# Kernel tuning notes

Measured on AMD Instinct MI355X. Metric: run time of the kernel, lower is better.

## Reference

```python
import jax, jax.numpy as jnp
import numpy as np

B, C, F, K = 16, 1000, 256, 10
IPM_ITERS = 20   # fixed-iteration primal-dual interior point (qpth eps=0.01 analogue)
SIGMA = 0.1      # centering parameter
MARGIN = 0.05


def setup_inputs() -> dict:
    key = jax.random.key(0)
    ks = jax.random.split(key, 6)
    logits_pred = jax.random.normal(ks[0], (B, C), jnp.float32)
    feats_pred = jax.random.normal(ks[1], (B, F), jnp.float32)
    feats_pred_0 = jax.random.normal(ks[2], (B, F), jnp.float32)
    head_W = jax.random.normal(ks[3], (C, F), jnp.float32) * 0.05
    head_bias = jax.random.normal(ks[4], (C,), jnp.float32) * 0.05
    # K distinct attack-target classes per sample (order defines the desired ranking)
    perm = jax.vmap(lambda k: jax.random.permutation(k, C))(jax.random.split(ks[5], B))
    attack_targets = perm[:, :K].astype(jnp.int32)
    margin = jnp.full((1,), MARGIN, jnp.float32)
    return {"logits_pred": logits_pred, "feats_pred": feats_pred,
            "feats_pred_0": feats_pred_0, "attack_targets": attack_targets,
            "head_W": head_W, "head_bias": head_bias, "margin": margin}


def build_D(attack_targets):
    # replicates the torch scatter/index_put sequence, in the same overwrite order
    col = jnp.arange(C)
    t_last = attack_targets[:, -1]
    base = -jnp.eye(C, dtype=jnp.float32)[None]                       # (B,C,C) via broadcast
    D = jnp.where(col[None, None, :] == t_last[:, None, None], 1.0, base)
    row_mask = (jnp.arange(C)[None, :, None] == attack_targets[:, None, :]).any(-1)  # (B,C)
    D = jnp.where(row_mask[:, :, None], 0.0, D)
    bi = jnp.broadcast_to(jnp.arange(B)[:, None], (B, K - 1))
    t_pos = attack_targets[:, :-1]
    t_neg = attack_targets[:, 1:]
    D = D.at[bi, t_neg, t_neg].set(-1.0)
    D = D.at[bi, t_neg, t_pos].set(1.0)
    return D


def solve_qp_ipm(p, G, h):
    # min_z z'z + p'z  s.t. G z <= h   (Q = 2*I), infeasible-start primal-dual IPM
    Bn, m, n = G.shape
    z = -0.5 * p                       # unconstrained minimizer (anchor feats)
    s = jnp.ones((Bn, m), p.dtype)
    lam = jnp.ones((Bn, m), p.dtype)
    eye_n = jnp.eye(n, dtype=p.dtype)
    big = jnp.asarray(1e10, p.dtype)

    def step(carry, _):
        z, lam, s = carry
        mu = (lam * s).mean(-1, keepdims=True)
        rd = 2.0 * z + p + jnp.einsum('bm,bmn->bn', lam, G)
        rp = jnp.einsum('bmn,bn->bm', G, z) + s - h
        rc = lam * s - SIGMA * mu
        w = lam / s
        M = 2.0 * eye_n + jnp.einsum('bmi,bm,bmj->bij', G, w, G)   # (B,n,n) KKT Schur
        rhs = -(rd + jnp.einsum('bmi,bm->bi', G, (lam * rp - rc) / s))
        dz = jnp.linalg.solve(M, rhs[..., None])[..., 0]
        ds = -rp - jnp.einsum('bmn,bn->bm', G, dz)
        dlam = -(rc + lam * ds) / s
        a1 = jnp.where(ds < 0, -s / ds, big).min(-1)
        a2 = jnp.where(dlam < 0, -lam / dlam, big).min(-1)
        alpha = jnp.minimum(1.0, 0.99 * jnp.minimum(a1, a2))[:, None]
        return (z + alpha * dz, lam + alpha * dlam, s + alpha * ds), None

    (z, lam, s), _ = jax.lax.scan(step, (z, lam, s), None, length=IPM_ITERS)
    return z


def reference(logits_pred, feats_pred, feats_pred_0, attack_targets, head_W, head_bias, margin):
    D = build_D(attack_targets)                                   # (B,C,C)
    G = -jnp.einsum('bck,kf->bcf', D, head_W)                     # (B,C,F)
    Hc = jnp.einsum('bck,k->bc', D, head_bias) - margin[0]        # = -(margin - D@b)
    Hc = Hc.at[jnp.arange(B), attack_targets[:, 0]].set(0.0)
    P = -2.0 * feats_pred
    z_sol = solve_qp_ipm(P, G, Hc)
    loss = ((feats_pred - z_sol) ** 2).sum(-1)                    # (B,)
    return loss
```

## Files before the change

### kernel.cpp

```cpp
#include <hip/hip_runtime.h>


#define B_N 16
#define C_N 1000
#define F_N 256
#define ITERS_N 20
#define SIGMA_C 0.1f
#define BIGV 1e10f

static const size_t OFF_WT  = 0;
static const size_t OFF_X   = 256000;
static const size_t OFF_M64 = 4352000;
static const size_t OFF_H   = 6449152;
static const size_t OFF_LAM = OFF_H   + 16000;
static const size_t OFF_S   = OFF_LAM + 16000;
static const size_t OFF_RP  = OFF_S   + 16000;
static const size_t OFF_RC  = OFF_RP  + 16000;
static const size_t OFF_WV  = OFF_RC  + 16000;
static const size_t OFF_Z   = OFF_WV  + 16000;
static const size_t OFF_DZ  = OFF_Z   + 4096;
static const size_t OFF_RHS = OFF_DZ  + 4096;
static const size_t OFF_AI  = OFF_RHS + 4096;
static const size_t OFF_BI  = OFF_AI  + 16000;

__device__ __forceinline__ float bsum256(float v, float* red) {
#pragma unroll
  for (int o = 32; o > 0; o >>= 1) v += __shfl_down(v, o);
  __syncthreads();
  if ((threadIdx.x & 63) == 0) red[threadIdx.x >> 6] = v;
  __syncthreads();
  return red[0] + red[1] + red[2] + red[3];
}
__device__ __forceinline__ float bmin256(float v, float* red) {
#pragma unroll
  for (int o = 32; o > 0; o >>= 1) v = fminf(v, __shfl_down(v, o));
  __syncthreads();
  if ((threadIdx.x & 63) == 0) red[threadIdx.x >> 6] = v;
  __syncthreads();
  return fminf(fminf(red[0], red[1]), fminf(red[2], red[3]));
}

__global__ __launch_bounds__(256) void k_transpose(const float* __restrict__ W,
                                                   float* __restrict__ WT) {
  __shared__ float tile[64][65];
  int tc = blockIdx.x & 15, tk = blockIdx.x >> 4;
  int c0 = tc * 64, k0 = tk * 64;
  int t = threadIdx.x;
  int jj = t & 63, r4 = t >> 6;
#pragma unroll
  for (int i = 0; i < 16; ++i) {
    int r = r4 + i * 4;
    int c = c0 + r;
    tile[r][jj] = (c < C_N) ? W[c * F_N + k0 + jj] : 0.f;
  }
  __syncthreads();
#pragma unroll
  for (int i = 0; i < 16; ++i) {
    int kr = r4 + i * 4;
    int cc = c0 + jj;
    if (cc < C_N) WT[(k0 + kr) * C_N + cc] = tile[jj][kr];
  }
}

__global__ __launch_bounds__(256) void k_setup(const int* __restrict__ tg,
                                               const float* __restrict__ bias,
                                               const float* __restrict__ feats,
                                               const float* __restrict__ marg,
                                               float* wsf) {
  int b = blockIdx.x, t = threadIdx.x;
  __shared__ int tsh[10];
  if (t < 10) tsh[t] = tg[b * 10 + t];
  __syncthreads();
  float m = marg[0];
  int t9 = tsh[9];
  float bias_t9 = bias[t9];
  int*   ai  = (int*)(wsf + OFF_AI) + b * C_N;
  int*   bi  = (int*)(wsf + OFF_BI) + b * C_N;
  float* h   = wsf + OFF_H   + b * C_N;
  float* lam = wsf + OFF_LAM + b * C_N;
  float* s   = wsf + OFF_S   + b * C_N;
#pragma unroll
  for (int r = 0; r < 4; ++r) {
    int c = t + 256 * r;
    if (c < C_N) {
      int rk = -1;
#pragma unroll
      for (int i = 0; i < 10; ++i) if (c == tsh[i]) rk = i;
      int av, bv; float hv;
      if (rk < 0)       { av = c;        bv = t9;         hv = bias_t9 - bias[c] - m; }
      else if (rk == 0) { av = 0;        bv = 0;          hv = 0.f; }
      else              { av = tsh[rk];  bv = tsh[rk-1];  hv = bias[tsh[rk-1]] - bias[tsh[rk]] - m; }
      ai[c] = av; bi[c] = bv; h[c] = hv; lam[c] = 1.f; s[c] = 1.f;
    }
  }
  (wsf + OFF_Z)[b * F_N + t] = feats[b * F_N + t];
}

__global__ __launch_bounds__(256) void k_buildX(const float* __restrict__ W,
                                                float* wsf) {
  int bb = blockIdx.x >> 3, part = blockIdx.x & 7;
  int t = threadIdx.x;
  __shared__ int aL[125], bL[125];
  int c0 = part * 125;
  const int* ai = (const int*)(wsf + OFF_AI) + bb * C_N;
  const int* bi = (const int*)(wsf + OFF_BI) + bb * C_N;
  if (t < 125) { aL[t] = ai[c0 + t]; bL[t] = bi[c0 + t]; }
  __syncthreads();
  float* X = wsf + OFF_X + (size_t)bb * 256000 + (size_t)c0 * F_N;
  for (int i = 0; i < 125; ++i) {
    float wa = W[aL[i] * F_N + t];
    float wb = W[bL[i] * F_N + t];
    X[i * F_N + t] = wa - wb;
  }
}

__global__ __launch_bounds__(256) void k_iter_pre(const float* __restrict__ W,
                                                  const float* __restrict__ feats,
                                                  const int* __restrict__ tg,
                                                  float* wsf, int do_update) {
  int b = blockIdx.x, t = threadIdx.x;
  __shared__ float zs[256], dzs[256];
  __shared__ __align__(16) float ys[1000];
  __shared__ float vs[1000];
  __shared__ float red[4];
  __shared__ int tsh[10];

  const float* WT = wsf + OFF_WT;
  const int* ai  = (const int*)(wsf + OFF_AI) + b * C_N;
  const int* bi  = (const int*)(wsf + OFF_BI) + b * C_N;
  float* h    = wsf + OFF_H   + b * C_N;
  float* lam  = wsf + OFF_LAM + b * C_N;
  float* s    = wsf + OFF_S   + b * C_N;
  float* rp   = wsf + OFF_RP  + b * C_N;
  float* rc   = wsf + OFF_RC  + b * C_N;
  float* wbuf = wsf + OFF_WV  + b * C_N;
  float* z    = wsf + OFF_Z   + b * F_N;
  float* dz   = wsf + OFF_DZ  + b * F_N;
  float* rhs  = wsf + OFF_RHS + b * F_N;

  if (t < 10) tsh[t] = tg[b * 10 + t];
  zs[t] = z[t];
  if (do_update) dzs[t] = dz[t];
  __syncthreads();

  float lamr[4], sr[4], rpr[4];
  if (do_update) {
    if (t < 250) {
      float4 acc = make_float4(0.f, 0.f, 0.f, 0.f);
      const float4* WT4 = (const float4*)WT;
#pragma unroll 4
      for (int k = 0; k < 256; ++k) {
        float zk = dzs[k];
        float4 w4 = WT4[k * 250 + t];
        acc.x += zk * w4.x; acc.y += zk * w4.y; acc.z += zk * w4.z; acc.w += zk * w4.w;
      }
      *(float4*)&ys[4 * t] = acc;
    }
    __syncthreads();
    float amin = BIGV;
    float dsr[4], dlr[4];
#pragma unroll
    for (int r = 0; r < 4; ++r) {
      int c = t + 256 * r;
      if (c < C_N) {
        float lv = lam[c], sv = s[c], rpv = rp[c], rcv = rc[c];
        float g = ys[ai[c]] - ys[bi[c]];
        float dsv = -rpv - g;
        float dlv = -(rcv + lv * dsv) / sv;
        if (dsv < 0.f) amin = fminf(amin, -sv / dsv);
        if (dlv < 0.f) amin = fminf(amin, -lv / dlv);
        lamr[r] = lv; sr[r] = sv; dsr[r] = dsv; dlr[r] = dlv;
      }
    }
    float am = bmin256(amin, red);
    float alpha = fminf(1.f, 0.99f * am);
#pragma unroll
    for (int r = 0; r < 4; ++r) {
      int c = t + 256 * r;
      if (c < C_N) {
        lamr[r] += alpha * dlr[r];
        sr[r]   += alpha * dsr[r];
        lam[c] = lamr[r]; s[c] = sr[r];
      }
    }
    zs[t] += alpha * dzs[t];
    z[t] = zs[t];
    __syncthreads();
  } else {
#pragma unroll
    for (int r = 0; r < 4; ++r) {
      int c = t + 256 * r;
      if (c < C_N) { lamr[r] = lam[c]; sr[r] = s[c]; }
    }
  }

  if (t < 250) {
    float4 acc = make_float4(0.f, 0.f, 0.f, 0.f);
    const float4* WT4 = (const float4*)WT;
#pragma unroll 4
    for (int k = 0; k < 256; ++k) {
      float zk = zs[k];
      float4 w4 = WT4[k * 250 + t];
      acc.x += zk * w4.x; acc.y += zk * w4.y; acc.z += zk * w4.z; acc.w += zk * w4.w;
    }
    *(float4*)&ys[4 * t] = acc;
  }
  __syncthreads();

  float musum = 0.f;
#pragma unroll
  for (int r = 0; r < 4; ++r) {
    int c = t + 256 * r;
    if (c < C_N) {
      float g = ys[ai[c]] - ys[bi[c]];
      rpr[r] = g + sr[r] - h[c];
      musum += lamr[r] * sr[r];
    }
  }
  float mu = bsum256(musum, red) * (1.f / 1000.f);

  float vsum = 0.f;
#pragma unroll
  for (int r = 0; r < 4; ++r) {
    int c = t + 256 * r;
    if (c < C_N) {
      float prod = lamr[r] * sr[r];
      float rcv = prod - SIGMA_C * mu;
      rc[c] = rcv; rp[c] = rpr[r];
      wbuf[c] = lamr[r] / sr[r];
      float vv = lamr[r] + (lamr[r] * rpr[r] - rcv) / sr[r];
      vs[c] = vv; vsum += vv;
    }
  }
  float S_all = bsum256(vsum, red);

  float vt[10];
#pragma unroll
  for (int i = 0; i < 10; ++i) vt[i] = vs[tsh[i]];
  float S_tgt = 0.f;
#pragma unroll
  for (int i = 0; i < 10; ++i) S_tgt += vt[i];
  float S_gen = S_all - S_tgt;
  __syncthreads();

#pragma unroll
  for (int r = 0; r < 4; ++r) {
    int c = t + 256 * r;
    if (c < C_N) {
      int rk = -1;
#pragma unroll
      for (int i = 0; i < 10; ++i) if (c == tsh[i]) rk = i;
      float vc = vs[c];
      float u;
      if (rk < 0)        u = vc;
      else if (rk == 0)  u = -vt[1];
      else if (rk < 9)   u = vc - vt[rk + 1];
      else               u = vc - S_gen;
      vs[c] = u;
    }
  }
  __syncthreads();

  {
    float acc = 0.f;
#pragma unroll 4
    for (int c = 0; c < C_N; ++c) acc += vs[c] * W[c * F_N + t];
    rhs[t] = -(2.f * zs[t] - 2.f * feats[b * F_N + t] + acc);
  }
}

__global__ __launch_bounds__(256) void k_syrk(float* wsf) {
  int blk = blockIdx.x;
  int b = blk / 10, tile = blk % 10;
  const int TI[10] = {0,1,1,2,2,2,3,3,3,3};
  const int TJ[10] = {0,0,1,0,1,2,0,1,2,3};
  int ti = TI[tile], tj = TJ[tile];
  int t = threadIdx.x;
  int tx = t & 15, ty = t >> 4;
  __shared__ __align__(16) float As[64][64];
  __shared__ __align__(16) float Bs[64][64];
  const float* X  = wsf + OFF_X  + (size_t)b * 256000;
  const float* wv = wsf + OFF_WV + b * C_N;
  float acc[4][4] = {{0.f}};
  int f4 = t & 15, jr0 = t >> 4;
  for (int cc = 0; cc < C_N; cc += 64) {
    __syncthreads();
#pragma unroll
    for (int rep = 0; rep < 4; ++rep) {
      int j = jr0 + rep * 16;
      int c = cc + j;
      float wj = (c < C_N) ? wv[c] : 0.f;
      float4 v = (c < C_N) ? *(const float4*)&X[(size_t)c * F_N + ti * 64 + f4 * 4]
                           : make_float4(0.f, 0.f, 0.f, 0.f);
      float4 u;
      if (tj == ti) u = v;
      else u = (c < C_N) ? *(const float4*)&X[(size_t)c * F_N + tj * 64 + f4 * 4]
                         : make_float4(0.f, 0.f, 0.f, 0.f);
      float4 vw = make_float4(wj * v.x, wj * v.y, wj * v.z, wj * v.w);
      *(float4*)&As[j][f4 * 4] = vw;
      *(float4*)&Bs[j][f4 * 4] = u;
    }
    __syncthreads();
#pragma unroll 4
    for (int j = 0; j < 64; ++j) {
      float4 a4 = *(const float4*)&As[j][tx * 4];
      float4 b4 = *(const float4*)&Bs[j][ty * 4];
      acc[0][0] += a4.x * b4.x; acc[0][1] += a4.x * b4.y; acc[0][2] += a4.x * b4.z; acc[0][3] += a4.x * b4.w;
      acc[1][0] += a4.y * b4.x; acc[1][1] += a4.y * b4.y; acc[1][2] += a4.y * b4.z; acc[1][3] += a4.y * b4.w;
      acc[2][0] += a4.z * b4.x; acc[2][1] += a4.z * b4.y; acc[2][2] += a4.z * b4.z; acc[2][3] += a4.z * b4.w;
      acc[3][0] += a4.w * b4.x; acc[3][1] += a4.w * b4.y; acc[3][2] += a4.w * b4.z; acc[3][3] += a4.w * b4.w;
    }
  }
  double* M64 = (double*)(wsf + OFF_M64) + (size_t)b * 65536;
#pragma unroll
  for (int e = 0; e < 4; ++e) {
    int i = ti * 64 + tx * 4 + e;
    int k0 = tj * 64 + ty * 4;
#pragma unroll
    for (int q = 0; q < 4; ++q) {
      float v = acc[e][q] + ((i == k0 + q) ? 2.f : 0.f);
      M64[(size_t)i * F_N + k0 + q] = (double)v;
    }
  }
}

__global__ __launch_bounds__(1024, 4) void k_chol(float* wsf) {
  int b = blockIdx.x, t = threadIdx.x;
  double* M = (double*)(wsf + OFF_M64) + (size_t)b * 65536;
  __shared__ double Sm[8464];
  double* Db   = Sm;
  double* invd = Sm + 272;
  double* Pb   = Sm + 304;
  double* Pu   = Sm + 4384;
  __shared__ double yv[256];
  __shared__ double red2[16 * 65];

  for (int p = 0; p < 16; ++p) {
    int p0 = p * 16, p1 = p0 + 16, nb = 256 - p1;

    if (t < 16) {
      int l = t;
      double a[16];
#pragma unroll
      for (int q = 0; q < 16; ++q) a[q] = M[(size_t)(p0 + l) * F_N + p0 + q];
#pragma unroll
      for (int j = 0; j < 16; ++j) {
        double d = __shfl(a[j], j);
        double dc = (fabs(d) < 1e-30) ? (d < 0.0 ? -1e-30 : 1e-30) : d;
        double inv = 1.0 / dc;
        if (l == j) a[j] = dc;
        else if (l > j) a[j] *= inv;
#pragma unroll
        for (int k = j + 1; k < 16; ++k) {
          double lkj = __shfl(a[j], k);
          if (l >= k) a[k] -= a[j] * (lkj * dc);
        }
      }
#pragma unroll
      for (int q = 0; q < 16; ++q) {
        M[(size_t)(p0 + l) * F_N + p0 + q] = a[q];
        Db[l * 17 + q] = a[q];
      }
      invd[l] = 1.0 / a[l];
    }
    __syncthreads();

    if (t < nb) {
      int r = p1 + t;
      double x[16];
#pragma unroll
      for (int q = 0; q < 16; ++q) x[q] = M[(size_t)r * F_N + p0 + q];
#pragma unroll
      for (int k = 0; k < 16; ++k) {
        double uk = x[k];
#pragma unroll
        for (int j = k + 1; j < 16; ++j) x[j] -= uk * Db[j * 17 + k];
        x[k] = uk * invd[k];
        Pu[t * 17 + k] = uk;
        Pb[t * 17 + k] = x[k];
      }
#pragma unroll
      for (int q = 0; q < 16; ++q) M[(size_t)r * F_N + p0 + q] = x[q];
    }
    __syncthreads();

    int nt4 = nb >> 2;
    int Ntile = nt4 * (nt4 + 1) / 2;
    for (int tt = t; tt < Ntile; tt += 1024) {
      float fsq = sqrtf((float)(8 * tt + 1));
      int ti = (int)((fsq - 1.f) * 0.5f);
      while ((ti + 1) * (ti + 2) / 2 <= tt) ++ti;
      while (ti * (ti + 1) / 2 > tt) --ti;
      int tk = tt - ti * (ti + 1) / 2;
      int ib = ti * 4, kb = tk * 4;
      double* m0 = M + (size_t)(p1 + ib) * F_N + p1 + kb;
      double a00 = m0[0],   a01 = m0[1],   a02 = m0[2],   a03 = m0[3];
      double a10 = m0[256], a11 = m0[257], a12 = m0[258], a13 = m0[259];
      double a20 = m0[512], a21 = m0[513], a22 = m0[514], a23 = m0[515];
      double a30 = m0[768], a31 = m0[769], a32 = m0[770], a33 = m0[771];
#pragma unroll
      for (int j = 0; j < 16; ++j) {
        double A0 = Pb[(ib + 0) * 17 + j], A1 = Pb[(ib + 1) * 17 + j];
        double A2 = Pb[(ib + 2) * 17 + j], A3 = Pb[(ib + 3) * 17 + j];
        double B0 = Pu[(kb + 0) * 17 + j], B1 = Pu[(kb + 1) * 17 + j];
        double B2 = Pu[(kb + 2) * 17 + j], B3 = Pu[(kb + 3) * 17 + j];
        a00 -= A0 * B0; a01 -= A0 * B1; a02 -= A0 * B2; a03 -= A0 * B3;
        a10 -= A1 * B0; a11 -= A1 * B1; a12 -= A1 * B2; a13 -= A1 * B3;
        a20 -= A2 * B0; a21 -= A2 * B1; a22 -= A2 * B2; a23 -= A2 * B3;
        a30 -= A3 * B0; a31 -= A3 * B1; a32 -= A3 * B2; a33 -= A3 * B3;
      }
      m0[0]   = a00; m0[1]   = a01; m0[2]   = a02; m0[3]   = a03;
      m0[256] = a10; m0[257] = a11; m0[258] = a12; m0[259] = a13;
      m0[512] = a20; m0[513] = a21; m0[514] = a22; m0[515] = a23;
      m0[768] = a30; m0[769] = a31; m0[770] = a32; m0[771] = a33;
    }
    __syncthreads();
  }

  {
    const float* rhs = wsf + OFF_RHS + (size_t)b * F_N;
    if (t < 256) yv[t] = (double)rhs[t];
  }
  __syncthreads();
  double* Ls = Sm;

  for (int blk = 0; blk < 4; ++blk) {
    int r0 = blk * 64;
    {
      int row = t >> 4, c4 = (t & 15) * 4;
#pragma unroll
      for (int q = 0; q < 4; ++q)
        Ls[row * 66 + c4 + q] = M[(size_t)(r0 + row) * F_N + r0 + c4 + q];
    }
    __syncthreads();
    if (t < 64) {
      int l = t;
      double acc = yv[r0 + l];
#pragma unroll
      for (int j = 0; j < 64; ++j) {
        double xj = __shfl(acc, j);
        if (l > j) acc -= Ls[l * 66 + j] * xj;
      }
      yv[r0 + l] = acc;
    }
    __syncthreads();
    int nrem = 192 - blk * 64;
    if (t < nrem) {
      int r = r0 + 64 + t;
      double a2 = 0.0;
#pragma unroll 4
      for (int j = 0; j < 64; ++j) a2 += M[(size_t)r * F_N + r0 + j] * yv[r0 + j];
      yv[r] -= a2;
    }
    __syncthreads();
  }

  if (t < 256) yv[t] = yv[t] / M[(size_t)t * F_N + t];
  __syncthreads();

  for (int blk = 3; blk >= 0; --blk) {
    int r0 = blk * 64, r1 = r0 + 64;
    if (blk < 3) {
      int i = r0 + (t & 63), g = t >> 6;
      double part = 0.0;
      for (int j = r1 + g; j < 256; j += 16) part += M[(size_t)j * F_N + i] * yv[j];
      red2[g * 65 + (t & 63)] = part;
      __syncthreads();
      if (t < 64) {
        double tot = 0.0;
#pragma unroll
        for (int g2 = 0; g2 < 16; ++g2) tot += red2[g2 * 65 + t];
        yv[r0 + t] -= tot;
      }
      __syncthreads();
    }
    {
      int row = t >> 4, c4 = (t & 15) * 4;
#pragma unroll
      for (int q = 0; q < 4; ++q)
        Ls[row * 66 + c4 + q] = M[(size_t)(r0 + row) * F_N + r0 + c4 + q];
    }
    __syncthreads();
    if (t < 64) {
      int l = t;
      double acc = yv[r0 + l];
#pragma unroll
      for (int j = 63; j >= 0; --j) {
        double xj = __shfl(acc, j);
        if (l < j) acc -= Ls[j * 66 + l] * xj;
      }
      yv[r0 + l] = acc;
    }
    __syncthreads();
  }

  if (t < 256) (wsf + OFF_DZ)[(size_t)b * F_N + t] = (float)yv[t];
}

__global__ __launch_bounds__(256) void k_final(const float* __restrict__ feats,
                                               float* wsf, float* __restrict__ out) {
  int b = blockIdx.x, t = threadIdx.x;
  __shared__ float zs[256], dzs[256];
  __shared__ __align__(16) float ys[1000];
  __shared__ float red[4];
  const float* WT = wsf + OFF_WT;
  const int* ai  = (const int*)(wsf + OFF_AI) + b * C_N;
  const int* bi  = (const int*)(wsf + OFF_BI) + b * C_N;
  const float* lam = wsf + OFF_LAM + b * C_N;
  const float* s   = wsf + OFF_S   + b * C_N;
  const float* rp  = wsf + OFF_RP  + b * C_N;
  const float* rc  = wsf + OFF_RC  + b * C_N;
  const float* z   = wsf + OFF_Z   + b * F_N;
  const float* dz  = wsf + OFF_DZ  + b * F_N;

  zs[t] = z[t];
  dzs[t] = dz[t];
  __syncthreads();
  if (t < 250) {
    float4 acc = make_float4(0.f, 0.f, 0.f, 0.f);
    const float4* WT4 = (const float4*)WT;
#pragma unroll 4
    for (int k = 0; k < 256; ++k) {
      float zk = dzs[k];
      float4 w4 = WT4[k * 250 + t];
      acc.x += zk * w4.x; acc.y += zk * w4.y; acc.z += zk * w4.z; acc.w += zk * w4.w;
    }
    *(float4*)&ys[4 * t] = acc;
  }
  __syncthreads();
  float amin = BIGV;
#pragma unroll
  for (int r = 0; r < 4; ++r) {
    int c = t + 256 * r;
    if (c < C_N) {
      float lv = lam[c], sv = s[c], rpv = rp[c], rcv = rc[c];
      float g = ys[ai[c]] - ys[bi[c]];
      float dsv = -rpv - g;
      float dlv = -(rcv + lv * dsv) / sv;
      if (dsv < 0.f) amin = fminf(amin, -sv / dsv);
      if (dlv < 0.f) amin = fminf(amin, -lv / dlv);
    }
  }
  float am = bmin256(amin, red);
  float alpha = fminf(1.f, 0.99f * am);
  float zf = zs[t] + alpha * dzs[t];
  float d = feats[b * F_N + t] - zf;
  float loss = bsum256(d * d, red);
  if (t == 0) out[b] = loss;
}

extern "C" void kernel_launch(void* const* d_in, const int* in_sizes, int n_in,
                              void* d_out, int out_size, void* d_ws, size_t ws_size,
                              hipStream_t stream) {
  (void)in_sizes; (void)n_in; (void)out_size; (void)ws_size;
  const float* feats = (const float*)d_in[1];
  const int*   tg    = (const int*)d_in[3];
  const float* W     = (const float*)d_in[4];
  const float* bias  = (const float*)d_in[5];
  const float* marg  = (const float*)d_in[6];
  float* wsf = (float*)d_ws;
  float* out = (float*)d_out;

  k_transpose<<<64, 256, 0, stream>>>(W, wsf + OFF_WT);
  k_setup<<<B_N, 256, 0, stream>>>(tg, bias, feats, marg, wsf);
  k_buildX<<<B_N * 8, 256, 0, stream>>>(W, wsf);
  for (int it = 0; it < ITERS_N; ++it) {
    k_iter_pre<<<B_N, 256, 0, stream>>>(W, feats, tg, wsf, it > 0 ? 1 : 0);
    k_syrk<<<B_N * 10, 256, 0, stream>>>(wsf);
    k_chol<<<B_N, 1024, 0, stream>>>(wsf);
  }
  k_final<<<B_N, 256, 0, stream>>>(feats, wsf, out);
}
```

Baseline: 8.466 ms.

## Overlap Cholesky panel factorization with trailing update via lookahead and double-buffered panels

Restructures the blocked LDL/Cholesky in k_chol to use lookahead. The next panel's column blocks are updated first, then the diagonal factorization and the triangular solve run on a few threads while the remaining threads update the rest of the trailing matrix. Panel buffers and inverse diagonals are double-buffered. Only the unscaled panel is stored, with the D^-1 scaling applied on the fly and an XOR swizzle on shared-memory rows to reduce bank conflicts. The aim is to cut the serial latency of the small diag/trsm phases, at the cost of more complex work partitioning and some extra multiplies in the update.

```diff
diff --git a/kernel.cpp b/kernel.cpp
--- a/kernel.cpp
+++ b/kernel.cpp
@@ -324,95 +324,142 @@
   }
 }
 
+#define PUROW(P, r, j) (P)[(r) * 17 + ((j) ^ ((r) & 7))]
+
+__device__ __forceinline__ void diag16(double* M, int P0d, double* Db,
+                                       double* invd) {
+  int l = threadIdx.x;
+  double a[16];
+#pragma unroll
+  for (int q = 0; q < 16; ++q) a[q] = M[(size_t)(P0d + l) * F_N + P0d + q];
+#pragma unroll
+  for (int j = 0; j < 16; ++j) {
+    double d = __shfl(a[j], j);
+    double dc = (fabs(d) < 1e-30) ? (d < 0.0 ? -1e-30 : 1e-30) : d;
+    double inv = 1.0 / dc;
+    if (l == j) a[j] = dc;
+    else if (l > j) a[j] *= inv;
+#pragma unroll
+    for (int k = j + 1; k < 16; ++k) {
+      double lkj = __shfl(a[j], k);
+      if (l >= k) a[k] -= a[j] * (lkj * dc);
+    }
+  }
+#pragma unroll
+  for (int q = 0; q < 16; ++q) {
+    M[(size_t)(P0d + l) * F_N + P0d + q] = a[q];
+    Db[l * 17 + q] = a[q];
+  }
+  invd[l] = 1.0 / a[l];
+}
+
+__device__ __forceinline__ void trsm16(double* M, int P0d, int tr,
+                                       const double* Db, const double* invd,
+                                       double* PuB) {
+  int r = P0d + 16 + tr;
+  double x[16];
+#pragma unroll
+  for (int q = 0; q < 16; ++q) x[q] = M[(size_t)r * F_N + P0d + q];
+#pragma unroll
+  for (int k = 0; k < 16; ++k) {
+    double uk = x[k];
+#pragma unroll
+    for (int j = k + 1; j < 16; ++j) x[j] -= uk * Db[j * 17 + k];
+    x[k] = uk * invd[k];
+    PUROW(PuB, tr, k) = uk;
+  }
+#pragma unroll
+  for (int q = 0; q < 16; ++q) M[(size_t)r * F_N + P0d + q] = x[q];
+}
+
+__device__ __forceinline__ void ldl_tile(double* M, const double* Pc,
+                                         const double* ic, int P1,
+                                         int ti, int tk) {
+  int ib = ti * 4, kb = tk * 4;
+  double* m0 = M + (size_t)(P1 + ib) * F_N + P1 + kb;
+  double a00 = m0[0],   a01 = m0[1],   a02 = m0[2],   a03 = m0[3];
+  double a10 = m0[256], a11 = m0[257], a12 = m0[258], a13 = m0[259];
+  double a20 = m0[512], a21 = m0[513], a22 = m0[514], a23 = m0[515];
+  double a30 = m0[768], a31 = m0[769], a32 = m0[770], a33 = m0[771];
+#pragma unroll
+  for (int j = 0; j < 16; ++j) {
+    double dj = ic[j];
+    double A0 = PUROW(Pc, ib + 0, j) * dj;
+    double A1 = PUROW(Pc, ib + 1, j) * dj;
+    double A2 = PUROW(Pc, ib + 2, j) * dj;
+    double A3 = PUROW(Pc, ib + 3, j) * dj;
+    double B0 = PUROW(Pc, kb + 0, j);
+    double B1 = PUROW(Pc, kb + 1, j);
+    double B2 = PUROW(Pc, kb + 2, j);
+    double B3 = PUROW(Pc, kb + 3, j);
+    a00 -= A0 * B0; a01 -= A0 * B1; a02 -= A0 * B2; a03 -= A0 * B3;
+    a10 -= A1 * B0; a11 -= A1 * B1; a12 -= A1 * B2; a13 -= A1 * B3;
+    a20 -= A2 * B0; a21 -= A2 * B1; a22 -= A2 * B2; a23 -= A2 * B3;
+    a30 -= A3 * B0; a31 -= A3 * B1; a32 -= A3 * B2; a33 -= A3 * B3;
+  }
+  m0[0]   = a00; m0[1]   = a01; m0[2]   = a02; m0[3]   = a03;
+  m0[256] = a10; m0[257] = a11; m0[258] = a12; m0[259] = a13;
+  m0[512] = a20; m0[513] = a21; m0[514] = a22; m0[515] = a23;
+  m0[768] = a30; m0[769] = a31; m0[770] = a32; m0[771] = a33;
+}
+
+__device__ __forceinline__ int2 trimap(int q) {
+  float fsq = sqrtf((float)(8 * q + 1));
+  int ti = (int)((fsq - 1.f) * 0.5f);
+  while ((ti + 1) * (ti + 2) / 2 <= q) ++ti;
+  while (ti * (ti + 1) / 2 > q) --ti;
+  return make_int2(ti, q - ti * (ti + 1) / 2);
+}
+
 __global__ __launch_bounds__(1024, 4) void k_chol(float* wsf) {
   int b = blockIdx.x, t = threadIdx.x;
   double* M = (double*)(wsf + OFF_M64) + (size_t)b * 65536;
   __shared__ double Sm[8464];
-  double* Db   = Sm;
-  double* invd = Sm + 272;
-  double* Pb   = Sm + 304;
-  double* Pu   = Sm + 4384;
   __shared__ double yv[256];
   __shared__ double red2[16 * 65];
-
-  for (int p = 0; p < 16; ++p) {
-    int p0 = p * 16, p1 = p0 + 16, nb = 256 - p1;
+  double* Db    = Sm;
+  double* invd2 = Sm + 272;
+  double* Pu    = Sm + 304;
+
+  if (t < 16) diag16(M, 0, Db, invd2);
+  __syncthreads();
+  if (t < 240) trsm16(M, 0, t, Db, invd2, Pu);
+  __syncthreads();
+
+  for (int p = 0; p < 15; ++p) {
+    int P1 = 16 * (p + 1);
+    int nt4 = (256 - P1) >> 2;
+    int m = nt4 - 4;
+    int N2 = m * (m + 1) / 2;
+    int Q = N2 > 768 ? N2 - 768 : 0;
+    int cur = p & 1, nxt = (p + 1) & 1;
+    const double* Pc = Pu + cur * 4080;
+    const double* ic = invd2 + cur * 16;
+
+    for (int q = t; q < 4 * nt4; q += 1024) {
+      int ti = q >> 2, tk = q & 3;
+      if (tk <= ti) ldl_tile(M, Pc, ic, P1, ti, tk);
+    }
+    __syncthreads();
 
     if (t < 16) {
-      int l = t;
-      double a[16];
-#pragma unroll
-      for (int q = 0; q < 16; ++q) a[q] = M[(size_t)(p0 + l) * F_N + p0 + q];
-#pragma unroll
-      for (int j = 0; j < 16; ++j) {
-        double d = __shfl(a[j], j);
-        double dc = (fabs(d) < 1e-30) ? (d < 0.0 ? -1e-30 : 1e-30) : d;
-        double inv = 1.0 / dc;
-        if (l == j) a[j] = dc;
-        else if (l > j) a[j] *= inv;
-#pragma unroll
-        for (int k = j + 1; k < 16; ++k) {
-          double lkj = __shfl(a[j], k);
-          if (l >= k) a[k] -= a[j] * (lkj * dc);
-        }
-      }
-#pragma unroll
-      for (int q = 0; q < 16; ++q) {
-        M[(size_t)(p0 + l) * F_N + p0 + q] = a[q];
-        Db[l * 17 + q] = a[q];
-      }
-      invd[l] = 1.0 / a[l];
-    }
-    __syncthreads();
-
-    if (t < nb) {
-      int r = p1 + t;
-      double x[16];
-#pragma unroll
-      for (int q = 0; q < 16; ++q) x[q] = M[(size_t)r * F_N + p0 + q];
-#pragma unroll
-      for (int k = 0; k < 16; ++k) {
-        double uk = x[k];
-#pragma unroll
-        for (int j = k + 1; j < 16; ++j) x[j] -= uk * Db[j * 17 + k];
-        x[k] = uk * invd[k];
-        Pu[t * 17 + k] = uk;
-        Pb[t * 17 + k] = x[k];
-      }
-#pragma unroll
-      for (int q = 0; q < 16; ++q) M[(size_t)r * F_N + p0 + q] = x[q];
-    }
-    __syncthreads();
-
-    int nt4 = nb >> 2;
-    int Ntile = nt4 * (nt4 + 1) / 2;
-    for (int tt = t; tt < Ntile; tt += 1024) {
-      float fsq = sqrtf((float)(8 * tt + 1));
-      int ti = (int)((fsq - 1.f) * 0.5f);
-      while ((ti + 1) * (ti + 2) / 2 <= tt) ++ti;
-      while (ti * (ti + 1) / 2 > tt) --ti;
-      int tk = tt - ti * (ti + 1) / 2;
-      int ib = ti * 4, kb = tk * 4;
-      double* m0 = M + (size_t)(p1 + ib) * F_N + p1 + kb;
-      double a00 = m0[0],   a01 = m0[1],   a02 = m0[2],   a03 = m0[3];
-      double a10 = m0[256], a11 = m0[257], a12 = m0[258], a13 = m0[259];
-      double a20 = m0[512], a21 = m0[513], a22 = m0[514], a23 = m0[515];
-      double a30 = m0[768], a31 = m0[769], a32 = m0[770], a33 = m0[771];
-#pragma unroll
-      for (int j = 0; j < 16; ++j) {
-        double A0 = Pb[(ib + 0) * 17 + j], A1 = Pb[(ib + 1) * 17 + j];
-        double A2 = Pb[(ib + 2) * 17 + j], A3 = Pb[(ib + 3) * 17 + j];
-        double B0 = Pu[(kb + 0) * 17 + j], B1 = Pu[(kb + 1) * 17 + j];
-        double B2 = Pu[(kb + 2) * 17 + j], B3 = Pu[(kb + 3) * 17 + j];
-        a00 -= A0 * B0; a01 -= A0 * B1; a02 -= A0 * B2; a03 -= A0 * B3;
-        a10 -= A1 * B0; a11 -= A1 * B1; a12 -= A1 * B2; a13 -= A1 * B3;
-        a20 -= A2 * B0; a21 -= A2 * B1; a22 -= A2 * B2; a23 -= A2 * B3;
-        a30 -= A3 * B0; a31 -= A3 * B1; a32 -= A3 * B2; a33 -= A3 * B3;
-      }
-      m0[0]   = a00; m0[1]   = a01; m0[2]   = a02; m0[3]   = a03;
-      m0[256] = a10; m0[257] = a11; m0[258] = a12; m0[259] = a13;
-      m0[512] = a20; m0[513] = a21; m0[514] = a22; m0[515] = a23;
-      m0[768] = a30; m0[769] = a31; m0[770] = a32; m0[771] = a33;
+      diag16(M, P1, Db, invd2 + nxt * 16);
+    } else if (t >= 64) {
+      for (int q = t - 64; q < Q; q += 960) {
+        int2 tt = trimap(q);
+        ldl_tile(M, Pc, ic, P1, tt.x + 4, tt.y + 4);
+      }
+    }
+    __syncthreads();
+
+    int nbn = 240 - P1;
+    if (t < nbn) {
+      trsm16(M, P1, t, Db, invd2 + nxt * 16, Pu + nxt * 4080);
+    } else if (t >= 256) {
+      for (int q = Q + (t - 256); q < N2; q += 768) {
+        int2 tt = trimap(q);
+        ldl_tile(M, Pc, ic, P1, tt.x + 4, tt.y + 4);
+      }
     }
     __syncthreads();
   }
```

Measured after the change: 11.28 ms. +33.2%, slower.
